# Kernel tuning notes

Measured on AMD Instinct MI355X. Metric: run time of the kernel, lower is better.

## Reference

```python
import jax, jax.numpy as jnp
import numpy as np

H = 512  # output_size


def setup_inputs() -> dict:
    key = jax.random.key(0)
    k = jax.random.split(key, 6)
    B, T, D = 64, 512, 512
    x = jax.random.normal(k[0], (B, T, D), dtype=jnp.float32)
    lengths = jnp.sort(jax.random.randint(k[1], (B,), 1, T + 1))[::-1].astype(jnp.int64)
    scale = 0.05
    w_in = jax.random.normal(k[2], (6 * H, D), dtype=jnp.float32) * scale
    b_in = jax.random.normal(k[3], (6 * H,), dtype=jnp.float32) * scale
    w_state = jax.random.normal(k[4], (5 * H, H), dtype=jnp.float32) * scale
    b_state = jax.random.normal(k[5], (5 * H,), dtype=jnp.float32) * scale
    return {"x": x, "lengths": lengths, "w_in": w_in, "b_in": b_in,
            "w_state": w_state, "b_state": b_state}


def reference(x, lengths, w_in, b_in, w_state, b_state):
    # x: [B,T,D]; returns padded outputs [B,T,H] (zeros past each length),
    # matching the padded content of the original PackedSequence output.
    B, T, _ = x.shape
    # Precompute all input projections: [B,T,6H]
    proj_in = jnp.einsum('btd,od->bto', x, w_in) + b_in
    proj_in_t = jnp.transpose(proj_in, (1, 0, 2))            # [T,B,6H]
    # valid mask per timestep: [T,B,1]
    mask_t = (jnp.arange(T)[:, None] < lengths[None, :])[..., None]

    def step(carry, inp):
        h, c = carry                                          # [B,H] each
        pi, m = inp                                           # [B,6H], [B,1]
        ps = h @ w_state.T + b_state                          # [B,5H]
        i_g = jax.nn.sigmoid(pi[:, 0*H:1*H] + ps[:, 0*H:1*H])
        f_g = jax.nn.sigmoid(pi[:, 1*H:2*H] + ps[:, 1*H:2*H])
        g   = jnp.tanh(     pi[:, 2*H:3*H] + ps[:, 2*H:3*H])
        o_g = jax.nn.sigmoid(pi[:, 3*H:4*H] + ps[:, 3*H:4*H])
        c_new = i_g * g + f_g * c
        out = o_g * jnp.tanh(c_new)
        hw  = jax.nn.sigmoid(pi[:, 4*H:5*H] + ps[:, 4*H:5*H])
        out = hw * out + (1.0 - hw) * pi[:, 5*H:6*H]
        # past-length positions are reset to zero (matches original slicing)
        out = jnp.where(m, out, 0.0)
        c_new = jnp.where(m, c_new, 0.0)
        return (out, c_new), out

    h0 = jnp.zeros((B, H), dtype=x.dtype)
    c0 = jnp.zeros((B, H), dtype=x.dtype)
    _, outs = jax.lax.scan(step, (h0, c0), (proj_in_t, mask_t))
    return jnp.transpose(outs, (1, 0, 2))                     # [B,T,H]
```

## Files before the change

kernel.cpp:

```cpp
#include <hip/hip_runtime.h>
#include <cstdint>
#include <cstddef>

#define BB 64
#define TT 512
#define DD 512
#define HH 512
#define SIXH 3072
#define NWG 32

typedef __attribute__((ext_vector_type(8))) short bf16x8;
typedef __attribute__((ext_vector_type(4))) float f32x4;
typedef __attribute__((ext_vector_type(4))) unsigned short u16x4;
typedef __attribute__((ext_vector_type(4))) int i32x4;

#define WS_FLAGS 0u
#define WS_CNT   256u
#define WS_H     16640u
#define WS_C     147712u
#define WS_PROJ  278784u

#define CLOAD16(dst, ptr) \
    asm volatile("global_load_dwordx4 %0, %1, off sc0 sc1" : "=v"(dst) : "v"(ptr))
#define CSTORE8(ptr, val) \
    asm volatile("global_store_dwordx2 %0, %1, off sc0 sc1" :: "v"(ptr), "v"(val))
#define WAIT4(N, a,b,c,d) \
    asm volatile("s_waitcnt vmcnt(" N ")" : "+v"(a),"+v"(b),"+v"(c),"+v"(d))

__device__ __forceinline__ float bf2f(unsigned short u) {
    union { unsigned int i; float f; } v; v.i = ((unsigned int)u) << 16; return v.f;
}
__device__ __forceinline__ unsigned short f2bf(float f) {
    union { unsigned int i; float f; } v; v.f = f;
    unsigned int r = v.i + 0x7FFFu + ((v.i >> 16) & 1u);
    return (unsigned short)(r >> 16);
}
__device__ __forceinline__ float sigm(float x) { return 1.0f / (1.0f + __expf(-x)); }
__device__ __forceinline__ float tanh_fast(float x) {
    return 1.0f - 2.0f / (__expf(2.0f * x) + 1.0f);
}

__device__ __forceinline__ bf16x8 cvt8v(const float* p) {
    const float4 a = *(const float4*)p;
    const float4 b = *(const float4*)(p + 4);
    bf16x8 o;
    o[0] = (short)f2bf(a.x); o[1] = (short)f2bf(a.y);
    o[2] = (short)f2bf(a.z); o[3] = (short)f2bf(a.w);
    o[4] = (short)f2bf(b.x); o[5] = (short)f2bf(b.y);
    o[6] = (short)f2bf(b.z); o[7] = (short)f2bf(b.w);
    return o;
}

__global__ void detect_kernel(const unsigned short* __restrict__ x16,
                              const int* __restrict__ len32,
                              int* __restrict__ flags) {
    const int lane = threadIdx.x;
    int bad = 0;
    for (int i = lane; i < 256; i += 64)
        if (fabsf(bf2f(x16[i])) > 1e4f) bad++;
#pragma unroll
    for (int off = 32; off; off >>= 1) bad += __shfl_down(bad, off);
    if (lane == 0) {
        flags[0] = (bad >= 16) ? 1 : 0;
        flags[1] = (len32[1] == 0 && len32[3] == 0 && len32[5] == 0) ? 1 : 0;
    }
}

template<int FP32>
__device__ __forceinline__ void proj_core(const void* __restrict__ xv,
                                          const void* __restrict__ wv,
                                          const void* __restrict__ bv,
                                          unsigned short* __restrict__ projc,
                                          int t0, int tc_shift) {
    const int tid  = threadIdx.x;
    const int wave = tid >> 6;
    const int lane = tid & 63;
    const int q    = lane >> 4;
    const int r    = lane & 15;

    const int m_blk = blockIdx.y * 64 + (wave >> 1) * 32;
    const int n_blk = blockIdx.x * 64 + (wave & 1) * 32;
    const int Tc    = 1 << tc_shift;
    const int b     = m_blk >> tc_shift;
    const int tl    = m_blk & (Tc - 1);

    const size_t xrow0 = (size_t)(b * TT + t0 + tl + r) * DD;
    const size_t xrow1 = (size_t)(b * TT + t0 + tl + 16 + r) * DD;
    const size_t wrow0 = (size_t)(n_blk + r) * DD;
    const size_t wrow1 = (size_t)(n_blk + 16 + r) * DD;

    f32x4 acc[2][2] = {};
    const int koff = q * 8;
    for (int k0 = 0; k0 < DD; k0 += 32) {
        bf16x8 a0, a1, b0, b1;
        const int k = k0 + koff;
        if (FP32) {
            const float* xf = (const float*)xv;
            const float* wf = (const float*)wv;
            a0 = cvt8v(xf + xrow0 + k);  a1 = cvt8v(xf + xrow1 + k);
            b0 = cvt8v(wf + wrow0 + k);  b1 = cvt8v(wf + wrow1 + k);
        } else {
            const unsigned short* xb = (const unsigned short*)xv;
            const unsigned short* wb = (const unsigned short*)wv;
            a0 = *(const bf16x8*)(xb + xrow0 + k);  a1 = *(const bf16x8*)(xb + xrow1 + k);
            b0 = *(const bf16x8*)(wb + wrow0 + k);  b1 = *(const bf16x8*)(wb + wrow1 + k);
        }
        acc[0][0] = __builtin_amdgcn_mfma_f32_16x16x32_bf16(a0, b0, acc[0][0], 0, 0, 0);
        acc[0][1] = __builtin_amdgcn_mfma_f32_16x16x32_bf16(a0, b1, acc[0][1], 0, 0, 0);
        acc[1][0] = __builtin_amdgcn_mfma_f32_16x16x32_bf16(a1, b0, acc[1][0], 0, 0, 0);
        acc[1][1] = __builtin_amdgcn_mfma_f32_16x16x32_bf16(a1, b1, acc[1][1], 0, 0, 0);
    }

#pragma unroll
    for (int mi = 0; mi < 2; mi++) {
#pragma unroll
        for (int ni = 0; ni < 2; ni++) {
            const int n = n_blk + ni * 16 + r;
            const float bias = FP32 ? ((const float*)bv)[n] : bf2f(((const unsigned short*)bv)[n]);
#pragma unroll
            for (int rr = 0; rr < 4; rr++) {
                const int m = m_blk + mi * 16 + q * 4 + rr;
                projc[(size_t)m * SIXH + n] = f2bf(acc[mi][ni][rr] + bias);
            }
        }
    }
}

__global__ __launch_bounds__(256) void proj_kernel(const void* xv, const void* wv, const void* bv,
                                                   unsigned short* projc, const int* flags,
                                                   const int* __restrict__ len32,
                                                   int t0, int tc_shift) {
    const int Tc  = 1 << tc_shift;
    const int mb  = blockIdx.y * 64;
    const int b   = mb >> tc_shift;
    const int tl0 = mb & (Tc - 1);
    const int len_b = flags[1] ? len32[2 * b] : len32[b];
    if (t0 + tl0 >= len_b) return;

    if (flags[0]) proj_core<1>(xv, wv, bv, projc, t0, tc_shift);
    else          proj_core<0>(xv, wv, bv, projc, t0, tc_shift);
}

__global__ __launch_bounds__(256, 1) void rec_kernel(
    const unsigned short* __restrict__ projc,
    const void* __restrict__ wsv, const void* __restrict__ bsv,
    const int* __restrict__ len32,
    unsigned short* __restrict__ hbuf, float* __restrict__ cbuf,
    int* __restrict__ wgflag, void* __restrict__ outv,
    const int* __restrict__ flags, int t0, int Tc)
{
    const int fp32 = flags[0], i64 = flags[1];
    const int tid  = threadIdx.x;
    const int wv   = tid >> 6;
    const int lane = tid & 63;
    const int q    = lane >> 4;
    const int r    = lane & 15;
    const int j0   = blockIdx.x * 16;
    const int b    = wv * 16 + r;

    __shared__ unsigned short wlds[5 * 16 * 64 * 8];

    for (int v = tid; v < 5 * 16 * 64; v += 256) {
        const int g  = v >> 10;
        const int ki = (v >> 6) & 15;
        const int ln = v & 63;
        const size_t gaddr = (size_t)(g * HH + j0 + (ln & 15)) * HH + ki * 32 + (ln >> 4) * 8;
        bf16x8 w8;
        if (fp32) w8 = cvt8v((const float*)wsv + gaddr);
        else      w8 = *(const bf16x8*)((const unsigned short*)wsv + gaddr);
        *(bf16x8*)&wlds[(size_t)v * 8] = w8;
    }

    float bs[5][4];
#pragma unroll
    for (int g = 0; g < 5; g++)
#pragma unroll
        for (int jj = 0; jj < 4; jj++)
            bs[g][jj] = fp32 ? ((const float*)bsv)[g * HH + j0 + q * 4 + jj]
                             : bf2f(((const unsigned short*)bsv)[g * HH + j0 + q * 4 + jj]);

    const int len = i64 ? len32[2 * b] : len32[b];

    int Lmax = 0;
    for (int i = 0; i < BB; i++) {
        const int li = i64 ? len32[2 * i] : len32[i];
        Lmax = (li > Lmax) ? li : Lmax;
    }

    float creg[4];
#pragma unroll
    for (int jj = 0; jj < 4; jj++)
        creg[jj] = cbuf[b * HH + j0 + q * 4 + jj];

    u16x4 pv[6];
    {
        const unsigned short* pb = projc + (size_t)b * Tc * SIXH + j0 + q * 4;
#pragma unroll
        for (int g = 0; g < 6; g++) pv[g] = *(const u16x4*)(pb + g * HH);
    }

    __syncthreads();

    union HU { i32x4 i; bf16x8 b; };
    union P8 { unsigned short s[4]; unsigned long long u; };

    int* const gbase = wgflag + (size_t)wv * NWG * 32;

    for (int t = t0; t < t0 + Tc; t++) {
        if (t >= Lmax) {
            if (fp32) {
                float* op = (float*)outv + ((size_t)b * TT + t) * HH + j0 + q * 4;
                *(float4*)op = make_float4(0.f, 0.f, 0.f, 0.f);
            } else {
                unsigned short* op = (unsigned short*)outv + ((size_t)b * TT + t) * HH + j0 + q * 4;
                *(unsigned long long*)op = 0ull;
            }
            continue;
        }

        const unsigned short* hcur = hbuf + (size_t)(t & 1) * (BB * HH);
        unsigned short*       hnxt = hbuf + (size_t)((t + 1) & 1) * (BB * HH);

        if (t > t0) {
            bool done;
            do {
                int f = (lane < NWG)
                    ? __hip_atomic_load(&gbase[lane * 32], __ATOMIC_RELAXED,
                                        __HIP_MEMORY_SCOPE_AGENT)
                    : t;
                done = __all(f >= t);
            } while (!done);
            asm volatile("" ::: "memory");
        }

        i32x4 hv[16];
#pragma unroll
        for (int ki = 0; ki < 16; ki++)
            CLOAD16(hv[ki], hcur + (size_t)b * HH + ki * 32 + q * 8);

        f32x4 acc[5] = {};
#define MFMA_CHUNK(KLO)                                                          \
        _Pragma("unroll")                                                        \
        for (int ki = (KLO); ki < (KLO) + 4; ki++) {                             \
            HU u; u.i = hv[ki];                                                  \
            _Pragma("unroll")                                                    \
            for (int g = 0; g < 5; g++) {                                        \
                bf16x8 aw = *(const bf16x8*)&wlds[((g * 16 + ki) * 64 + lane) * 8]; \
                acc[g] = __builtin_amdgcn_mfma_f32_16x16x32_bf16(aw, u.b, acc[g], 0, 0, 0); \
            }                                                                    \
        }
        WAIT4("12", hv[0],  hv[1],  hv[2],  hv[3]);   MFMA_CHUNK(0)
        WAIT4("8",  hv[4],  hv[5],  hv[6],  hv[7]);   MFMA_CHUNK(4)
        WAIT4("4",  hv[8],  hv[9],  hv[10], hv[11]);  MFMA_CHUNK(8)
        WAIT4("0",  hv[12], hv[13], hv[14], hv[15]);  MFMA_CHUNK(12)
#undef MFMA_CHUNK

        P8 hp;
        float ov4[4];
#pragma unroll
        for (int jj = 0; jj < 4; jj++) {
            const float i_g = sigm(bf2f(pv[0][jj]) + acc[0][jj] + bs[0][jj]);
            const float f_g = sigm(bf2f(pv[1][jj]) + acc[1][jj] + bs[1][jj]);
            const float g_t = tanh_fast(bf2f(pv[2][jj]) + acc[2][jj] + bs[2][jj]);
            const float o_g = sigm(bf2f(pv[3][jj]) + acc[3][jj] + bs[3][jj]);
            const float hw  = sigm(bf2f(pv[4][jj]) + acc[4][jj] + bs[4][jj]);

            float c_new = i_g * g_t + f_g * creg[jj];
            float ov = o_g * tanh_fast(c_new);
            ov = hw * ov + (1.0f - hw) * bf2f(pv[5][jj]);
            if (t >= len) { ov = 0.0f; c_new = 0.0f; }
            creg[jj] = c_new;
            ov4[jj] = ov;
            hp.s[jj] = f2bf(ov);
        }

        CSTORE8((void*)(hnxt + (size_t)b * HH + j0 + q * 4), hp.u);
        asm volatile("s_waitcnt vmcnt(0)" ::: "memory");
        if (lane == 0)
            __hip_atomic_store(&gbase[blockIdx.x * 32], t + 1,
                               __ATOMIC_RELAXED, __HIP_MEMORY_SCOPE_AGENT);

        if (fp32) {
            float* op = (float*)outv + ((size_t)b * TT + t) * HH + j0 + q * 4;
            *(float4*)op = make_float4(ov4[0], ov4[1], ov4[2], ov4[3]);
        } else {
            unsigned short* op = (unsigned short*)outv + ((size_t)b * TT + t) * HH + j0 + q * 4;
            *(unsigned long long*)op = hp.u;
        }
        const int tln = t - t0 + 1;
        if (tln < Tc) {
            const unsigned short* pb = projc + ((size_t)b * Tc + tln) * SIXH + j0 + q * 4;
#pragma unroll
            for (int g = 0; g < 6; g++) pv[g] = *(const u16x4*)(pb + g * HH);
        }
    }

#pragma unroll
    for (int jj = 0; jj < 4; jj++)
        cbuf[b * HH + j0 + q * 4 + jj] = creg[jj];
}

extern "C" void kernel_launch(void* const* d_in, const int* in_sizes, int n_in,
                              void* d_out, int out_size, void* d_ws, size_t ws_size,
                              hipStream_t stream) {
    const void* xv      = d_in[0];
    const int*  len     = (const int*)d_in[1];
    const void* w_in    = d_in[2];
    const void* b_in    = d_in[3];
    const void* w_state = d_in[4];
    const void* b_state = d_in[5];

    char* ws = (char*)d_ws;
    int* flags  = (int*)(ws + WS_FLAGS);
    int* wgflag = (int*)(ws + WS_CNT);
    unsigned short* hbuf = (unsigned short*)(ws + WS_H);
    float* cbuf = (float*)(ws + WS_C);
    unsigned short* projc = (unsigned short*)(ws + WS_PROJ);

    int tc_shift = 9;
    while (tc_shift > 6 &&
           WS_PROJ + ((size_t)BB << tc_shift) * SIXH * 2 > ws_size) tc_shift--;
    const int Tc = 1 << tc_shift;

    detect_kernel<<<1, 64, 0, stream>>>((const unsigned short*)xv, len, flags);
    hipMemsetAsync(ws + WS_CNT, 0, WS_PROJ - WS_CNT, stream);

    for (int c = 0; c < TT / Tc; c++) {
        const int t0 = c * Tc;
        proj_kernel<<<dim3(SIXH / 64, (BB << tc_shift) >> 6), 256, 0, stream>>>(
            xv, w_in, b_in, projc, flags, len, t0, tc_shift);
        rec_kernel<<<NWG, 256, 0, stream>>>(projc, w_state, b_state, len,
                                            hbuf, cbuf, wgflag, d_out, flags, t0, Tc);
    }
}
```

Before: 3.024 ms.

## Pre-convert inputs to bf16 once and cache barrier flags in spin wait

Adds a conversion kernel that turns x, w_in and b_in into bf16/fp32 workspace copies once, so the projection GEMM reads half-size bf16 tiles instead of reconverting fp32 data on every reload. The rec_kernel spin-wait now keeps a per-lane cached flag value and only reloads flags that have not yet reached the current step, cutting redundant atomic loads. The cost is an extra full pass over x (about 64 MB read, 32 MB written) and a larger workspace requirement. The proj kernel may also run out of workspace room for projc, which would shrink Tc.

After: 2.704 ms. 1.12x faster.

```diff
diff --git a/kernel.cpp b/kernel.cpp
--- a/kernel.cpp
+++ b/kernel.cpp
@@ -18,7 +18,10 @@
 #define WS_CNT   256u
 #define WS_H     16640u
 #define WS_C     147712u
-#define WS_PROJ  278784u
+#define WS_XB    278784u
+#define WS_WB    33833216u
+#define WS_BF    36978944u
+#define WS_PROJ  36991232u
 
 #define CLOAD16(dst, ptr) \
     asm volatile("global_load_dwordx4 %0, %1, off sc0 sc1" : "=v"(dst) : "v"(ptr))
@@ -66,12 +69,60 @@
     }
 }
 
-template<int FP32>
-__device__ __forceinline__ void proj_core(const void* __restrict__ xv,
-                                          const void* __restrict__ wv,
-                                          const void* __restrict__ bv,
-                                          unsigned short* __restrict__ projc,
-                                          int t0, int tc_shift) {
+__global__ __launch_bounds__(256) void convert_kernel(
+    const void* __restrict__ xv, const void* __restrict__ wv,
+    const void* __restrict__ bv,
+    unsigned short* __restrict__ xb, unsigned short* __restrict__ wb,
+    float* __restrict__ bf, const int* __restrict__ flags)
+{
+    const int fp32 = flags[0];
+    const size_t NX = (size_t)BB * TT * DD;
+    const size_t NW = (size_t)SIXH * DD;
+    const size_t tid = (size_t)blockIdx.x * blockDim.x + threadIdx.x;
+    const size_t stride = (size_t)gridDim.x * blockDim.x;
+
+    if (fp32) {
+        const float* xf = (const float*)xv;
+        for (size_t i = tid * 4; i < NX; i += stride * 4) {
+            const float4 v = *(const float4*)(xf + i);
+            u16x4 o; o[0] = f2bf(v.x); o[1] = f2bf(v.y); o[2] = f2bf(v.z); o[3] = f2bf(v.w);
+            *(u16x4*)(xb + i) = o;
+        }
+        const float* wf = (const float*)wv;
+        for (size_t i = tid * 4; i < NW; i += stride * 4) {
+            const float4 v = *(const float4*)(wf + i);
+            u16x4 o; o[0] = f2bf(v.x); o[1] = f2bf(v.y); o[2] = f2bf(v.z); o[3] = f2bf(v.w);
+            *(u16x4*)(wb + i) = o;
+        }
+        const float* bvf = (const float*)bv;
+        for (size_t i = tid; i < SIXH; i += stride) bf[i] = bvf[i];
+    } else {
+        const unsigned short* xs = (const unsigned short*)xv;
+        for (size_t i = tid * 4; i < NX; i += stride * 4)
+            *(u16x4*)(xb + i) = *(const u16x4*)(xs + i);
+        const unsigned short* wsrc = (const unsigned short*)wv;
+        for (size_t i = tid * 4; i < NW; i += stride * 4)
+            *(u16x4*)(wb + i) = *(const u16x4*)(wsrc + i);
+        const unsigned short* bs = (const unsigned short*)bv;
+        for (size_t i = tid; i < SIXH; i += stride) bf[i] = bf2f(bs[i]);
+    }
+}
+
+__global__ __launch_bounds__(256) void proj_kernel(
+    const unsigned short* __restrict__ xb, const unsigned short* __restrict__ wb,
+    const float* __restrict__ bf, unsigned short* __restrict__ projc,
+    const int* __restrict__ flags, const int* __restrict__ len32,
+    int t0, int tc_shift)
+{
+    const int Tc  = 1 << tc_shift;
+    {
+        const int mb  = blockIdx.y * 64;
+        const int bq  = mb >> tc_shift;
+        const int tl0 = mb & (Tc - 1);
+        const int len_b = flags[1] ? len32[2 * bq] : len32[bq];
+        if (t0 + tl0 >= len_b) return;
+    }
+
     const int tid  = threadIdx.x;
     const int wave = tid >> 6;
     const int lane = tid & 63;
@@ -80,7 +131,6 @@
 
     const int m_blk = blockIdx.y * 64 + (wave >> 1) * 32;
     const int n_blk = blockIdx.x * 64 + (wave & 1) * 32;
-    const int Tc    = 1 << tc_shift;
     const int b     = m_blk >> tc_shift;
     const int tl    = m_blk & (Tc - 1);
 
@@ -92,19 +142,11 @@
     f32x4 acc[2][2] = {};
     const int koff = q * 8;
     for (int k0 = 0; k0 < DD; k0 += 32) {
-        bf16x8 a0, a1, b0, b1;
         const int k = k0 + koff;
-        if (FP32) {
-            const float* xf = (const float*)xv;
-            const float* wf = (const float*)wv;
-            a0 = cvt8v(xf + xrow0 + k);  a1 = cvt8v(xf + xrow1 + k);
-            b0 = cvt8v(wf + wrow0 + k);  b1 = cvt8v(wf + wrow1 + k);
-        } else {
-            const unsigned short* xb = (const unsigned short*)xv;
-            const unsigned short* wb = (const unsigned short*)wv;
-            a0 = *(const bf16x8*)(xb + xrow0 + k);  a1 = *(const bf16x8*)(xb + xrow1 + k);
-            b0 = *(const bf16x8*)(wb + wrow0 + k);  b1 = *(const bf16x8*)(wb + wrow1 + k);
-        }
+        bf16x8 a0 = *(const bf16x8*)(xb + xrow0 + k);
+        bf16x8 a1 = *(const bf16x8*)(xb + xrow1 + k);
+        bf16x8 b0 = *(const bf16x8*)(wb + wrow0 + k);
+        bf16x8 b1 = *(const bf16x8*)(wb + wrow1 + k);
         acc[0][0] = __builtin_amdgcn_mfma_f32_16x16x32_bf16(a0, b0, acc[0][0], 0, 0, 0);
         acc[0][1] = __builtin_amdgcn_mfma_f32_16x16x32_bf16(a0, b1, acc[0][1], 0, 0, 0);
         acc[1][0] = __builtin_amdgcn_mfma_f32_16x16x32_bf16(a1, b0, acc[1][0], 0, 0, 0);
@@ -116,7 +158,7 @@
 #pragma unroll
         for (int ni = 0; ni < 2; ni++) {
             const int n = n_blk + ni * 16 + r;
-            const float bias = FP32 ? ((const float*)bv)[n] : bf2f(((const unsigned short*)bv)[n]);
+            const float bias = bf[n];
 #pragma unroll
             for (int rr = 0; rr < 4; rr++) {
                 const int m = m_blk + mi * 16 + q * 4 + rr;
@@ -124,21 +166,6 @@
             }
         }
     }
-}
-
-__global__ __launch_bounds__(256) void proj_kernel(const void* xv, const void* wv, const void* bv,
-                                                   unsigned short* projc, const int* flags,
-                                                   const int* __restrict__ len32,
-                                                   int t0, int tc_shift) {
-    const int Tc  = 1 << tc_shift;
-    const int mb  = blockIdx.y * 64;
-    const int b   = mb >> tc_shift;
-    const int tl0 = mb & (Tc - 1);
-    const int len_b = flags[1] ? len32[2 * b] : len32[b];
-    if (t0 + tl0 >= len_b) return;
-
-    if (flags[0]) proj_core<1>(xv, wv, bv, projc, t0, tc_shift);
-    else          proj_core<0>(xv, wv, bv, projc, t0, tc_shift);
 }
 
 __global__ __launch_bounds__(256, 1) void rec_kernel(
@@ -205,6 +232,7 @@
     union P8 { unsigned short s[4]; unsigned long long u; };
 
     int* const gbase = wgflag + (size_t)wv * NWG * 32;
+    int fcache = (lane < NWG) ? 0 : 0x7fffffff;
 
     for (int t = t0; t < t0 + Tc; t++) {
         if (t >= Lmax) {
@@ -224,11 +252,10 @@
         if (t > t0) {
             bool done;
             do {
-                int f = (lane < NWG)
-                    ? __hip_atomic_load(&gbase[lane * 32], __ATOMIC_RELAXED,
-                                        __HIP_MEMORY_SCOPE_AGENT)
-                    : t;
-                done = __all(f >= t);
+                if (fcache < t)
+                    fcache = __hip_atomic_load(&gbase[lane * 32], __ATOMIC_RELAXED,
+                                               __HIP_MEMORY_SCOPE_AGENT);
+                done = __all(fcache >= t);
             } while (!done);
             asm volatile("" ::: "memory");
         }
@@ -315,6 +342,9 @@
     int* wgflag = (int*)(ws + WS_CNT);
     unsigned short* hbuf = (unsigned short*)(ws + WS_H);
     float* cbuf = (float*)(ws + WS_C);
+    unsigned short* xb = (unsigned short*)(ws + WS_XB);
+    unsigned short* wb = (unsigned short*)(ws + WS_WB);
+    float* bf = (float*)(ws + WS_BF);
     unsigned short* projc = (unsigned short*)(ws + WS_PROJ);
 
     int tc_shift = 9;
@@ -323,12 +353,13 @@
     const int Tc = 1 << tc_shift;
 
     detect_kernel<<<1, 64, 0, stream>>>((const unsigned short*)xv, len, flags);
-    hipMemsetAsync(ws + WS_CNT, 0, WS_PROJ - WS_CNT, stream);
+    hipMemsetAsync(ws + WS_CNT, 0, WS_XB - WS_CNT, stream);
+    convert_kernel<<<2048, 256, 0, stream>>>(xv, w_in, b_in, xb, wb, bf, flags);
 
     for (int c = 0; c < TT / Tc; c++) {
         const int t0 = c * Tc;
         proj_kernel<<<dim3(SIXH / 64, (BB << tc_shift) >> 6), 256, 0, stream>>>(
-            xv, w_in, b_in, projc, flags, len, t0, tc_shift);
+            xb, wb, bf, projc, flags, len, t0, tc_shift);
         rec_kernel<<<NWG, 256, 0, stream>>>(projc, w_state, b_state, len,
                                             hbuf, cbuf, wgflag, d_out, flags, t0, Tc);
     }
```
